# Kernel optimization log

Measured on AMD Instinct MI355X. Metric: run time of the kernel, lower is better.

The kernel has to match this reference:

```python
import jax, jax.numpy as jnp
import numpy as np

D_MODEL = 1024
D_STATE = 16
EXPAND = 2
D_INNER = D_MODEL * EXPAND
DT_RANK = D_MODEL // 16


def setup_inputs() -> dict:
    key = jax.random.key(0)
    ks = jax.random.split(key, 12)
    B, T = 2, 2048
    s_in = 1.0 / np.sqrt(D_MODEL)
    s_x = 1.0 / np.sqrt(D_INNER)
    s_dt = 1.0 / np.sqrt(DT_RANK)
    inp = {
        'u': jax.random.normal(ks[0], (B, T, D_MODEL), jnp.float32),
        'W_in': jax.random.uniform(ks[1], (2 * D_INNER, D_MODEL), jnp.float32, -s_in, s_in),
        'b_in': jax.random.uniform(ks[2], (2 * D_INNER,), jnp.float32, -s_in, s_in),
        'W_x': jax.random.uniform(ks[3], (DT_RANK + 2 * D_STATE, D_INNER), jnp.float32, -s_x, s_x),
        'b_x': jax.random.uniform(ks[4], (DT_RANK + 2 * D_STATE,), jnp.float32, -s_x, s_x),
        'W_dt': jax.random.uniform(ks[5], (D_INNER, DT_RANK), jnp.float32, -s_dt, s_dt),
        'b_dt': jax.random.uniform(ks[6], (D_INNER,), jnp.float32, -s_dt, s_dt),
        'A_log': jnp.log(jnp.abs(jax.random.normal(ks[7], (D_INNER, D_STATE), jnp.float32)) + 1e-6),
        'D': jnp.ones((D_INNER,), jnp.float32),
        'W_out': jax.random.uniform(ks[8], (D_MODEL, D_INNER), jnp.float32, -s_x, s_x),
        'b_out': jax.random.uniform(ks[9], (D_MODEL,), jnp.float32, -s_x, s_x),
    }
    return inp


def _ssm_forward(u, W_in, b_in, W_x, b_x, W_dt, b_dt, A_log, D, W_out, b_out):
    B, T, _ = u.shape
    u_inner = u @ W_in.T + b_in                       # [B,T,2*d_inner]
    x, z = jnp.split(u_inner, 2, axis=-1)             # each [B,T,d_inner]
    dbc = x @ W_x.T + b_x                             # [B,T,dt_rank+2N]
    delta_raw = dbc[..., :DT_RANK]
    B_ssm = dbc[..., DT_RANK:DT_RANK + D_STATE]       # [B,T,N]
    C_ssm = dbc[..., DT_RANK + D_STATE:]              # [B,T,N]
    delta = jax.nn.softplus(delta_raw @ W_dt.T + b_dt)  # [B,T,d_inner]
    A = -jnp.exp(A_log)                               # [d_inner,N]

    def step(h, xs):
        dt_t, x_t, Bt, Ct = xs                        # [B,d], [B,d], [B,N], [B,N]
        dA = jnp.exp(dt_t[..., None] * A)             # [B,d,N]
        dB = dt_t[..., None] * Bt[:, None, :]         # [B,d,N]
        h = h * dA + x_t[..., None] * dB
        y_t = jnp.einsum('bdn,bn->bd', h, Ct)
        return h, y_t

    h0 = jnp.zeros((B, D_INNER, D_STATE), u.dtype)
    xs = (jnp.swapaxes(delta, 0, 1), jnp.swapaxes(x, 0, 1),
          jnp.swapaxes(B_ssm, 0, 1), jnp.swapaxes(C_ssm, 0, 1))
    _, y = jax.lax.scan(step, h0, xs)                 # y: [T,B,d_inner]
    y = jnp.swapaxes(y, 0, 1)                         # [B,T,d_inner]
    y = y + x * D
    y = y * (z * jax.nn.sigmoid(z))                   # SiLU gate
    return y @ W_out.T + b_out                        # [B,T,d_model]


def reference(u, W_in, b_in, W_x, b_x, W_dt, b_dt, A_log, D, W_out, b_out):
    return _ssm_forward(u, W_in, b_in, W_x, b_x, W_dt, b_dt, A_log, D, W_out, b_out)
```

## Files before the change

### kernel.cpp

```cpp
#include <hip/hip_runtime.h>
#include <math.h>

#define BATCH 2
#define SEQ   2048
#define DM    1024
#define DI    2048
#define NST   16
#define MT    (BATCH*SEQ)
#define CHK   64
#define LCH   (SEQ/CHK)

typedef __attribute__((ext_vector_type(8))) short  bf16x8;
typedef __attribute__((ext_vector_type(4))) float  f32x4;

static __device__ __forceinline__ unsigned short f2bf(float f) {
  unsigned u = __float_as_uint(f);
  u += 0x7fff + ((u >> 16) & 1);
  return (unsigned short)(u >> 16);
}
static __device__ __forceinline__ float bf2f(unsigned short h) {
  return __uint_as_float(((unsigned)h) << 16);
}
static __device__ __forceinline__ float fexp2(float x) {
  float r;
  asm("v_exp_f32 %0, %1" : "=v"(r) : "v"(x));
  return r;
}
static __device__ __forceinline__ float flog2(float x) {
  float r;
  asm("v_log_f32 %0, %1" : "=v"(r) : "v"(x));
  return r;
}

#define SEG_U    (MT*DM/4)
#define SEG_WIN  (2*DI*DM/4)
#define SEG_WOUT (DM*DI/4)
#define SEG_WX   (96*DI/4)
#define SEG_WDT  (DI*64/4)
#define SEG_A    (DI*NST/4)
#define CUM0 SEG_U
#define CUM1 (CUM0+SEG_WIN)
#define CUM2 (CUM1+SEG_WOUT)
#define CUM3 (CUM2+SEG_WX)
#define CUM4 (CUM3+SEG_WDT)
#define CUM5 (CUM4+SEG_A)

__global__ __launch_bounds__(256) void convall_kernel(
    const float* __restrict__ u, const float* __restrict__ W_in,
    const float* __restrict__ W_out, const float* __restrict__ W_x,
    const float* __restrict__ W_dt, const float* __restrict__ A_log,
    unsigned short* __restrict__ u_bf, unsigned short* __restrict__ win_bf,
    unsigned short* __restrict__ wout_bf, unsigned short* __restrict__ wx_bf,
    unsigned short* __restrict__ wdt_bf, float* __restrict__ A2tab)
{
  const int gid = blockIdx.x*256 + threadIdx.x;
  const float4* src; ushort4* dst; int idx;
  if (gid < CUM0)      { idx = gid;        src = (const float4*)u;     dst = (ushort4*)u_bf; }
  else if (gid < CUM1) { idx = gid - CUM0; src = (const float4*)W_in;  dst = (ushort4*)win_bf; }
  else if (gid < CUM2) { idx = gid - CUM1; src = (const float4*)W_out; dst = (ushort4*)wout_bf; }
  else if (gid < CUM3) { idx = gid - CUM2; src = (const float4*)W_x;   dst = (ushort4*)wx_bf; }
  else if (gid < CUM4) { idx = gid - CUM3; src = (const float4*)W_dt;  dst = (ushort4*)wdt_bf; }
  else if (gid < CUM5) {
    int i = gid - CUM4;
    float4 v = ((const float4*)A_log)[i];
    float4 o;
    o.x = -1.44269504f * __expf(v.x);
    o.y = -1.44269504f * __expf(v.y);
    o.z = -1.44269504f * __expf(v.z);
    o.w = -1.44269504f * __expf(v.w);
    ((float4*)A2tab)[i] = o;
    return;
  } else return;
  float4 v = src[idx];
  ushort4 o;
  o.x = f2bf(v.x); o.y = f2bf(v.y); o.z = f2bf(v.z); o.w = f2bf(v.w);
  dst[idx] = o;
}

#define MEMFENCE asm volatile("" ::: "memory")

template<int K>
__global__ __launch_bounds__(512, 2) void gemm3_kernel(
    const unsigned short* __restrict__ A,
    const unsigned short* __restrict__ B,
    const float* __restrict__ bias,
    unsigned short* __restrict__ Cout, int nbx)
{
  extern __shared__ unsigned short smem[];
  unsigned short* As = smem;
  unsigned short* Bs = smem + 4*256*32;
  constexpr int NT = K / 32;

  const int nwg = gridDim.x;
  const int cpx = nwg >> 3;
  const int bid = blockIdx.x;
  const int swz = (bid & 7) * cpx + (bid >> 3);
  const int bx = swz % nbx;
  const int by = swz / nbx;

  const int tid  = threadIdx.x;
  const int lane = tid & 63;
  const int wid  = tid >> 6;
  const int wr   = wid >> 2;
  const int wc   = wid & 3;

  const size_t arow0 = (size_t)by * 256;
  const size_t brow0 = (size_t)bx * 256;

  const int s_r4 = lane >> 2;
  const int s_c  = lane & 3;

  auto STAGE_A = [&](int slot, int T) {
#pragma unroll
    for (int i = 0; i < 2; ++i) {
      const int r  = wid*32 + i*16 + s_r4;
      const int lc = s_c ^ ((r >> 1) & 3);
      const unsigned short* g = A + (arow0 + r)*(size_t)K + T*32 + lc*8;
      __builtin_amdgcn_global_load_lds(
          (const __attribute__((address_space(1))) void*)g,
          (__attribute__((address_space(3))) void*)(As + slot*(256*32) + (wid*32 + i*16)*32),
          16, 0, 0);
    }
  };
  auto STAGE_B = [&](int slot, int T) {
#pragma unroll
    for (int i = 0; i < 2; ++i) {
      const int r  = wid*32 + i*16 + s_r4;
      const int lc = s_c ^ ((r >> 1) & 3);
      const unsigned short* g = B + (brow0 + r)*(size_t)K + T*32 + lc*8;
      __builtin_amdgcn_global_load_lds(
          (const __attribute__((address_space(1))) void*)g,
          (__attribute__((address_space(3))) void*)(Bs + slot*(256*32) + (wid*32 + i*16)*32),
          16, 0, 0);
    }
  };

  f32x4 zero = {0.f, 0.f, 0.f, 0.f};
  f32x4 acc[8][4];
#pragma unroll
  for (int i = 0; i < 8; ++i)
#pragma unroll
    for (int j = 0; j < 4; ++j) acc[i][j] = zero;

  STAGE_A(0, 0); STAGE_B(0, 0);
  STAGE_A(1, 1); STAGE_B(1, 1);
  STAGE_A(2, 2); STAGE_B(2, 2);
  asm volatile("s_waitcnt vmcnt(8)" ::: "memory");
  __builtin_amdgcn_s_barrier();
  MEMFENCE;

  const int lrow = lane & 15, k8 = lane >> 4;
  bf16x8 bfr[4];

  for (int t = 0; t < NT; ++t) {
    const int slot = t & 3;
    const int sts  = (t + 3) & 3;
    const unsigned short* Asl = As + slot*(256*32);
    const unsigned short* Bsl = Bs + slot*(256*32);

    bf16x8 af[4];
#pragma unroll
    for (int nj = 0; nj < 4; ++nj) {
      const int r = wc*64 + nj*16 + lrow;
      bfr[nj] = *(const bf16x8*)&Bsl[r*32 + (k8 ^ ((r >> 1) & 3))*8];
    }
#pragma unroll
    for (int mi = 0; mi < 4; ++mi) {
      const int r = wr*128 + mi*16 + lrow;
      af[mi] = *(const bf16x8*)&Asl[r*32 + (k8 ^ ((r >> 1) & 3))*8];
    }
    if (t + 3 < NT) STAGE_A(sts, t + 3);
    MEMFENCE;
    __builtin_amdgcn_s_barrier();
    MEMFENCE;
    __builtin_amdgcn_s_setprio(1);
#pragma unroll
    for (int mi = 0; mi < 4; ++mi)
#pragma unroll
      for (int nj = 0; nj < 4; ++nj)
        acc[mi][nj] = __builtin_amdgcn_mfma_f32_16x16x32_bf16(
                          af[mi], bfr[nj], acc[mi][nj], 0, 0, 0);
    __builtin_amdgcn_s_setprio(0);
    MEMFENCE;
    __builtin_amdgcn_s_barrier();
    MEMFENCE;

#pragma unroll
    for (int mi = 0; mi < 4; ++mi) {
      const int r = wr*128 + 64 + mi*16 + lrow;
      af[mi] = *(const bf16x8*)&Asl[r*32 + (k8 ^ ((r >> 1) & 3))*8];
    }
    if (t + 3 < NT) STAGE_B(sts, t + 3);
    MEMFENCE;
    __builtin_amdgcn_s_barrier();
    MEMFENCE;
    __builtin_amdgcn_s_setprio(1);
#pragma unroll
    for (int mi = 0; mi < 4; ++mi)
#pragma unroll
      for (int nj = 0; nj < 4; ++nj)
        acc[mi + 4][nj] = __builtin_amdgcn_mfma_f32_16x16x32_bf16(
                              af[mi], bfr[nj], acc[mi + 4][nj], 0, 0, 0);
    __builtin_amdgcn_s_setprio(0);

    if (t <= NT - 4)      asm volatile("s_waitcnt vmcnt(8)" ::: "memory");
    else if (t == NT - 3) asm volatile("s_waitcnt vmcnt(4)" ::: "memory");
    else                  asm volatile("s_waitcnt vmcnt(0)" ::: "memory");
    __builtin_amdgcn_s_barrier();
    MEMFENCE;
  }

  const int lcol = lane & 15, lrq = lane >> 4;
#pragma unroll
  for (int nj = 0; nj < 4; ++nj) {
    const int colg = bx*256 + wc*64 + nj*16 + lcol;
    const float bv = bias[colg];
#pragma unroll
    for (int mi = 0; mi < 8; ++mi) {
      const int rowg = by*256 + wr*128 + mi*16 + lrq*4;
#pragma unroll
      for (int q = 0; q < 4; ++q)
        Cout[(size_t)(rowg + q)*4096 + colg] = f2bf(acc[mi][nj][q] + bv);
    }
  }
}

template<int BN, int BK, bool OUT_BF16, int LDC, int ACT>
__global__ __launch_bounds__(256, 4) void gemm2_kernel(
    const unsigned short* __restrict__ A,
    const unsigned short* __restrict__ B,
    const float* __restrict__ bias,
    void* __restrict__ Cout, int K, int nbx)
{
  constexpr int NH = BK / 32;
  constexpr int NJ = BN / 32;
  __shared__ unsigned short Abuf[2][NH][128*32];
  __shared__ unsigned short Bbuf[2][NH][BN*32];

  const int nwg = gridDim.x;
  const int cpx = nwg >> 3;
  const int bid = blockIdx.x;
  const int swz = (bid & 7) * cpx + (bid >> 3);
  const int bx = swz % nbx;
  const int by = swz / nbx;

  const int tid  = threadIdx.x;
  const int lane = tid & 63;
  const int wid  = tid >> 6;
  const int wr   = wid >> 1;
  const int wc   = wid & 1;
  const int lr    = lane >> 2;
  const int lslot = lane & 3;

  f32x4 zero = {0.f, 0.f, 0.f, 0.f};
  f32x4 acc[4][NJ];
#pragma unroll
  for (int i = 0; i < 4; ++i)
#pragma unroll
    for (int j = 0; j < NJ; ++j) acc[i][j] = zero;

  const size_t arow0 = (size_t)by * 128;
  const size_t brow0 = (size_t)bx * BN;
  const int NT = K / BK;

  auto STAGE = [&](int buf, int k0) {
#pragma unroll
    for (int half = 0; half < NH; ++half) {
#pragma unroll
      for (int i = 0; i < 2; ++i) {
        const int Rb = (wid + i*4) * 16;
        const int r  = Rb + lr;
        const int c8 = lslot ^ ((r >> 1) & 3);
        const unsigned short* ga = A + (arow0 + r)*(size_t)K + k0 + half*32 + c8*8;
        __builtin_amdgcn_global_load_lds(
            (const __attribute__((address_space(1))) void*)ga,
            (__attribute__((address_space(3))) void*)(&Abuf[buf][half][Rb*32]),
            16, 0, 0);
      }
#pragma unroll
      for (int i = 0; i < BN/64; ++i) {
        const int Rb = (wid + i*4) * 16;
        const int r  = Rb + lr;
        const int c8 = lslot ^ ((r >> 1) & 3);
        const unsigned short* gb = B + (brow0 + r)*(size_t)K + k0 + half*32 + c8*8;
        __builtin_amdgcn_global_load_lds(
            (const __attribute__((address_space(1))) void*)gb,
            (__attribute__((address_space(3))) void*)(&Bbuf[buf][half][Rb*32]),
            16, 0, 0);
      }
    }
  };

  STAGE(0, 0);
  __syncthreads();

  const int lrow = lane & 15, k8 = lane >> 4;
  int cur = 0;
  for (int kt = 0; kt < NT; ++kt) {
    if (kt + 1 < NT) STAGE(cur ^ 1, (kt + 1) * BK);

#pragma unroll
    for (int half = 0; half < NH; ++half) {
      bf16x8 af[4], bfr[NJ];
#pragma unroll
      for (int mi = 0; mi < 4; ++mi) {
        const int r = wr*64 + mi*16 + lrow;
        af[mi] = *(const bf16x8*)&Abuf[cur][half][r*32 + (k8 ^ ((r >> 1) & 3))*8];
      }
#pragma unroll
      for (int nj = 0; nj < NJ; ++nj) {
        const int r = wc*(BN/2) + nj*16 + lrow;
        bfr[nj] = *(const bf16x8*)&Bbuf[cur][half][r*32 + (k8 ^ ((r >> 1) & 3))*8];
      }
      __builtin_amdgcn_s_setprio(1);
#pragma unroll
      for (int mi = 0; mi < 4; ++mi)
#pragma unroll
        for (int nj = 0; nj < NJ; ++nj)
          acc[mi][nj] = __builtin_amdgcn_mfma_f32_16x16x32_bf16(
                            af[mi], bfr[nj], acc[mi][nj], 0, 0, 0);
      __builtin_amdgcn_s_setprio(0);
    }
    __syncthreads();
    cur ^= 1;
  }

  const int lcol = lane & 15, lrq = lane >> 4;
#pragma unroll
  for (int nj = 0; nj < NJ; ++nj) {
    const int colg = bx*BN + wc*(BN/2) + nj*16 + lcol;
    const float bv = bias[colg];
#pragma unroll
    for (int mi = 0; mi < 4; ++mi) {
      const int rowg = by*128 + wr*64 + mi*16 + lrq*4;
#pragma unroll
      for (int q = 0; q < 4; ++q) {
        float v = acc[mi][nj][q] + bv;
        if constexpr (ACT == 1) {
          float e = fexp2(-1.44269504f * fabsf(v));
          v = fmaxf(v, 0.f) + 0.69314718f * flog2(1.f + e);
        }
        if constexpr (OUT_BF16)
          ((unsigned short*)Cout)[(size_t)(rowg + q)*LDC + colg] = f2bf(v);
        else
          ((float*)Cout)[(size_t)(rowg + q)*LDC + colg] = v;
      }
    }
  }
}

__global__ __launch_bounds__(256) void dbc_mfma_kernel(
    const unsigned short* __restrict__ A,
    const unsigned short* __restrict__ Bw,
    float* __restrict__ partial)
{
  __shared__ unsigned short Abuf[64*32];
  __shared__ unsigned short Bbuf[96*32];

  const int tid  = threadIdx.x;
  const int lane = tid & 63;
  const int wid  = tid >> 6;
  const int lr    = lane >> 2;
  const int lslot = lane & 3;
  const size_t arow0 = (size_t)blockIdx.x * 64;
  const int ks   = blockIdx.y;
  const int k0b  = ks * (DI/4);

  f32x4 zero = {0.f, 0.f, 0.f, 0.f};
  f32x4 acc[6];
#pragma unroll
  for (int j = 0; j < 6; ++j) acc[j] = zero;

  for (int k0 = k0b; k0 < k0b + DI/4; k0 += 32) {
    {
      const int Rb = wid*16;
      const int r  = Rb + lr;
      const int c8 = lslot ^ ((r >> 1) & 3);
      const unsigned short* ga = A + (arow0 + r)*4096 + k0 + c8*8;
      __builtin_amdgcn_global_load_lds(
          (const __attribute__((address_space(1))) void*)ga,
          (__attribute__((address_space(3))) void*)(Abuf + Rb*32), 16, 0, 0);
    }
    if (wid < 3) {
#pragma unroll
      for (int i = 0; i < 2; ++i) {
        const int Rb = wid*32 + i*16;
        const int r  = Rb + lr;
        const int c8 = lslot ^ ((r >> 1) & 3);
        const unsigned short* gb = Bw + (size_t)r*DI + k0 + c8*8;
        __builtin_amdgcn_global_load_lds(
            (const __attribute__((address_space(1))) void*)gb,
            (__attribute__((address_space(3))) void*)(Bbuf + Rb*32), 16, 0, 0);
      }
    }
    __syncthreads();

    const int lrow = lane & 15, k8 = lane >> 4;
    const int ra = wid*16 + lrow;
    bf16x8 af = *(const bf16x8*)&Abuf[ra*32 + (k8 ^ ((ra >> 1) & 3))*8];
#pragma unroll
    for (int nj = 0; nj < 6; ++nj) {
      const int rb = nj*16 + lrow;
      bf16x8 bf_ = *(const bf16x8*)&Bbuf[rb*32 + (k8 ^ ((rb >> 1) & 3))*8];
      acc[nj] = __builtin_amdgcn_mfma_f32_16x16x32_bf16(af, bf_, acc[nj], 0, 0, 0);
    }
    __syncthreads();
  }

  const int lcol = lane & 15, lrq = lane >> 4;
  const int rowg = (int)arow0 + wid*16 + lrq*4;
#pragma unroll
  for (int nj = 0; nj < 6; ++nj) {
    const int colg = nj*16 + lcol;
#pragma unroll
    for (int q = 0; q < 4; ++q)
      partial[((size_t)ks*MT + rowg + q)*96 + colg] = acc[nj][q];
  }
}

__global__ __launch_bounds__(256) void dbc_reduce_kernel(
    const float* __restrict__ partial, const float* __restrict__ bx,
    float* __restrict__ dbc, unsigned short* __restrict__ draw_bf)
{
  const int gid = blockIdx.x*256 + threadIdx.x;
  const int m = gid / 96;
  const int c = gid - m*96;
  const size_t stride = (size_t)MT*96;
  float s = partial[gid] + partial[gid + stride]
          + partial[gid + 2*stride] + partial[gid + 3*stride] + bx[c];
  if (c < 64) draw_bf[(size_t)m*64 + c] = f2bf(s);
  else        dbc[(size_t)m*96 + c] = s;
}

__global__ __launch_bounds__(256) void scanA_kernel(
    const unsigned short* __restrict__ uib,
    const float* __restrict__ dbc,
    const unsigned short* __restrict__ delta_bf,
    const float* __restrict__ A2tab,
    float* __restrict__ P,
    float* __restrict__ S)
{
  const int bid = blockIdx.x;
  const int d   = (bid & 7)*256 + threadIdx.x;
  const int c   = (bid >> 3) & (CHK-1);
  const int b   = bid >> 9;

  float A2[NST];
  {
    const float4* ap = (const float4*)(A2tab + (size_t)d*NST);
#pragma unroll
    for (int q = 0; q < 4; ++q) {
      float4 v = ap[q];
      A2[q*4+0] = v.x; A2[q*4+1] = v.y; A2[q*4+2] = v.z; A2[q*4+3] = v.w;
    }
  }

  float h[NST];
#pragma unroll
  for (int nn = 0; nn < NST; ++nn) h[nn] = 0.f;
  float sdt = 0.f;

  const int t0 = c * LCH;
  const unsigned short* dptr = delta_bf + ((size_t)b*SEQ + t0)*DI + d;
  const unsigned short* xptr = uib      + ((size_t)b*SEQ + t0)*4096 + d;
  const float* bptr          = dbc      + ((size_t)b*SEQ + t0)*96 + 64;

  float dt = bf2f(dptr[0]);
  float xv = bf2f(xptr[0]);
  float4 Bv0 = *(const float4*)(bptr + 0);
  float4 Bv1 = *(const float4*)(bptr + 4);
  float4 Bv2 = *(const float4*)(bptr + 8);
  float4 Bv3 = *(const float4*)(bptr + 12);

  for (int t = 0; t < LCH; ++t) {
    const float dtc = dt, xvc = xv;
    float Bc[NST] = {Bv0.x,Bv0.y,Bv0.z,Bv0.w, Bv1.x,Bv1.y,Bv1.z,Bv1.w,
                     Bv2.x,Bv2.y,Bv2.z,Bv2.w, Bv3.x,Bv3.y,Bv3.z,Bv3.w};
    if (t + 1 < LCH) {
      const size_t tn = (size_t)(t+1);
      dt = bf2f(dptr[tn*DI]);
      xv = bf2f(xptr[tn*4096]);
      const float* bp = bptr + tn*96;
      Bv0 = *(const float4*)(bp + 0);
      Bv1 = *(const float4*)(bp + 4);
      Bv2 = *(const float4*)(bp + 8);
      Bv3 = *(const float4*)(bp + 12);
    }
    sdt += dtc;
    const float xdt = xvc * dtc;
#pragma unroll
    for (int nn = 0; nn < NST; ++nn) {
      float dA = fexp2(dtc * A2[nn]);
      h[nn] = h[nn]*dA + xdt*Bc[nn];
    }
  }

  float* Pp = P + (((size_t)b*CHK + c)*DI + d)*NST;
  float* Sp = S + (((size_t)b*CHK + c)*DI + d)*NST;
#pragma unroll
  for (int q = 0; q < 4; ++q) {
    float4 pv = { fexp2(A2[q*4+0]*sdt), fexp2(A2[q*4+1]*sdt),
                  fexp2(A2[q*4+2]*sdt), fexp2(A2[q*4+3]*sdt) };
    float4 sv = { h[q*4+0], h[q*4+1], h[q*4+2], h[q*4+3] };
    *(float4*)(Pp + q*4) = pv;
    *(float4*)(Sp + q*4) = sv;
  }
}

__global__ __launch_bounds__(256) void scanB_kernel(
    const float* __restrict__ P, float* __restrict__ S)
{
  const int gid = blockIdx.x*256 + threadIdx.x;
  const int n4 = gid & 3;
  const int d  = (gid >> 2) & (DI-1);
  const int b  = gid >> 13;

  float4 h = {0.f, 0.f, 0.f, 0.f};
  for (int c = 0; c < CHK; ++c) {
    const size_t idx = (((size_t)b*CHK + c)*DI + d)*NST + n4*4;
    float4 p = *(const float4*)(P + idx);
    float4 s = *(const float4*)(S + idx);
    *(float4*)(S + idx) = h;
    h.x = h.x*p.x + s.x;
    h.y = h.y*p.y + s.y;
    h.z = h.z*p.z + s.z;
    h.w = h.w*p.w + s.w;
  }
}

__global__ __launch_bounds__(256) void scanC_kernel(
    const unsigned short* __restrict__ uib,
    const float* __restrict__ dbc,
    const unsigned short* __restrict__ delta_bf,
    const float* __restrict__ A2tab,
    const float* __restrict__ Dp,
    const float* __restrict__ S,
    unsigned short* __restrict__ y_bf)
{
  const int bid = blockIdx.x;
  const int d   = (bid & 7)*256 + threadIdx.x;
  const int c   = (bid >> 3) & (CHK-1);
  const int b   = bid >> 9;

  float A2[NST];
  {
    const float4* ap = (const float4*)(A2tab + (size_t)d*NST);
#pragma unroll
    for (int q = 0; q < 4; ++q) {
      float4 v = ap[q];
      A2[q*4+0] = v.x; A2[q*4+1] = v.y; A2[q*4+2] = v.z; A2[q*4+3] = v.w;
    }
  }
  const float Dv = Dp[d];

  float h[NST];
  {
    const float* Sp = S + (((size_t)b*CHK + c)*DI + d)*NST;
#pragma unroll
    for (int q = 0; q < 4; ++q) {
      float4 sv = *(const float4*)(Sp + q*4);
      h[q*4+0] = sv.x; h[q*4+1] = sv.y; h[q*4+2] = sv.z; h[q*4+3] = sv.w;
    }
  }

  const int t0 = c * LCH;
  const unsigned short* dptr = delta_bf + ((size_t)b*SEQ + t0)*DI + d;
  const unsigned short* xptr = uib      + ((size_t)b*SEQ + t0)*4096 + d;
  const float* cptr          = dbc      + ((size_t)b*SEQ + t0)*96;
  unsigned short* yp         = y_bf     + ((size_t)b*SEQ + t0)*DI + d;

  float dt = bf2f(dptr[0]);
  float xv = bf2f(xptr[0]);
  float zv = bf2f(xptr[2048]);
  float4 Bv0 = *(const float4*)(cptr + 64);
  float4 Bv1 = *(const float4*)(cptr + 68);
  float4 Bv2 = *(const float4*)(cptr + 72);
  float4 Bv3 = *(const float4*)(cptr + 76);
  float4 Cv0 = *(const float4*)(cptr + 80);
  float4 Cv1 = *(const float4*)(cptr + 84);
  float4 Cv2 = *(const float4*)(cptr + 88);
  float4 Cv3 = *(const float4*)(cptr + 92);

  for (int t = 0; t < LCH; ++t) {
    const float dtc = dt, xvc = xv, zvc = zv;
    float Bc[NST] = {Bv0.x,Bv0.y,Bv0.z,Bv0.w, Bv1.x,Bv1.y,Bv1.z,Bv1.w,
                     Bv2.x,Bv2.y,Bv2.z,Bv2.w, Bv3.x,Bv3.y,Bv3.z,Bv3.w};
    float Cc[NST] = {Cv0.x,Cv0.y,Cv0.z,Cv0.w, Cv1.x,Cv1.y,Cv1.z,Cv1.w,
                     Cv2.x,Cv2.y,Cv2.z,Cv2.w, Cv3.x,Cv3.y,Cv3.z,Cv3.w};
    if (t + 1 < LCH) {
      const size_t tn = (size_t)(t+1);
      dt = bf2f(dptr[tn*DI]);
      xv = bf2f(xptr[tn*4096]);
      zv = bf2f(xptr[tn*4096 + 2048]);
      const float* cp = cptr + tn*96;
      Bv0 = *(const float4*)(cp + 64);
      Bv1 = *(const float4*)(cp + 68);
      Bv2 = *(const float4*)(cp + 72);
      Bv3 = *(const float4*)(cp + 76);
      Cv0 = *(const float4*)(cp + 80);
      Cv1 = *(const float4*)(cp + 84);
      Cv2 = *(const float4*)(cp + 88);
      Cv3 = *(const float4*)(cp + 92);
    }
    const float xdt = xvc * dtc;
    float y = 0.f;
#pragma unroll
    for (int nn = 0; nn < NST; ++nn) {
      float dA = fexp2(dtc * A2[nn]);
      h[nn] = h[nn]*dA + xdt*Bc[nn];
      y += h[nn]*Cc[nn];
    }
    y += xvc * Dv;
    y *= zvc / (1.f + fexp2(-1.44269504f * zvc));
    yp[(size_t)t*DI] = f2bf(y);
  }
}

extern "C" void kernel_launch(void* const* d_in, const int* in_sizes, int n_in,
                              void* d_out, int out_size, void* d_ws, size_t ws_size,
                              hipStream_t stream)
{
  const float* u     = (const float*)d_in[0];
  const float* W_in  = (const float*)d_in[1];
  const float* b_in  = (const float*)d_in[2];
  const float* W_x   = (const float*)d_in[3];
  const float* b_x   = (const float*)d_in[4];
  const float* W_dt  = (const float*)d_in[5];
  const float* b_dt  = (const float*)d_in[6];
  const float* A_log = (const float*)d_in[7];
  const float* Dp    = (const float*)d_in[8];
  const float* W_out = (const float*)d_in[9];
  const float* b_out = (const float*)d_in[10];
  float* out = (float*)d_out;

  unsigned short* ui_bf    = (unsigned short*)d_ws;
  float*          dbc      = (float*)(ui_bf + (size_t)MT*4096);
  unsigned short* delta_bf = (unsigned short*)(dbc + (size_t)MT*96);
  unsigned short* y_bf     = delta_bf + (size_t)MT*DI;
  unsigned short* wout_bf  = y_bf + (size_t)MT*DI;
  unsigned short* wx_bf    = wout_bf + (size_t)DM*DI;
  unsigned short* wdt_bf   = wx_bf + (size_t)96*DI;
  unsigned short* draw_bf  = wdt_bf + (size_t)DI*64;
  float*          S        = (float*)(draw_bf + (size_t)MT*64);
  float*          A2tab    = S + (size_t)BATCH*CHK*DI*NST;
  float*          partial  = A2tab + (size_t)DI*NST;

  unsigned short* u_bf   = (unsigned short*)d_out;
  unsigned short* win_bf = u_bf + (size_t)MT*DM;
  float* P = (float*)d_out;

  convall_kernel<<<CUM5/256, 256, 0, stream>>>(
      u, W_in, W_out, W_x, W_dt, A_log,
      u_bf, win_bf, wout_bf, wx_bf, wdt_bf, A2tab);

  bool big = hipFuncSetAttribute(
      (const void*)gemm3_kernel<DM>,
      hipFuncAttributeMaxDynamicSharedMemorySize, 131072) == hipSuccess;
  if (big) {
    gemm3_kernel<DM><<<16*16, 512, 131072, stream>>>(
        u_bf, win_bf, b_in, ui_bf, 16);
  } else {
    gemm2_kernel<128, 32, true, 4096, 0><<<32*32, 256, 0, stream>>>(
        u_bf, win_bf, b_in, ui_bf, DM, 32);
  }

  dbc_mfma_kernel<<<dim3(MT/64, 4), 256, 0, stream>>>(ui_bf, wx_bf, partial);
  dbc_reduce_kernel<<<MT*96/256, 256, 0, stream>>>(partial, b_x, dbc, draw_bf);

  gemm2_kernel<128, 32, true, 2048, 1><<<16*32, 256, 0, stream>>>(
      draw_bf, wdt_bf, b_dt, delta_bf, 64, 16);

  scanA_kernel<<<BATCH*CHK*DI/256, 256, 0, stream>>>(ui_bf, dbc, delta_bf, A2tab, P, S);
  scanB_kernel<<<BATCH*DI*4/256, 256, 0, stream>>>(P, S);
  scanC_kernel<<<BATCH*CHK*DI/256, 256, 0, stream>>>(ui_bf, dbc, delta_bf, A2tab, Dp, S, y_bf);

  gemm2_kernel<64, 64, false, 1024, 0><<<16*32, 256, 0, stream>>>(
      y_bf, wout_bf, b_out, out, DI, 16);
}
```

Measured before the change: 185.5 us.

## Split-K the output projection GEMM and drop intermediate barriers in gemm3

The output projection now runs as a two-way split-K GEMM with 128x128 tiles. Each K half writes fp32 partials into workspace reused from the dead u_inner buffer, and a new vectorised kernel sums the halves and adds the bias. Separately, the mid-iteration LDS barriers in the main input GEMM are removed, keeping only the end-of-iteration barrier, to cut synchronisation stalls. The split-K path adds an extra round trip of fp32 partials through global memory. The barrier removal leans on the 4-slot ring buffer spacing to stay race-free.

```diff
diff --git a/kernel.cpp b/kernel.cpp
--- a/kernel.cpp
+++ b/kernel.cpp
@@ -171,8 +171,6 @@
     }
     if (t + 3 < NT) STAGE_A(sts, t + 3);
     MEMFENCE;
-    __builtin_amdgcn_s_barrier();
-    MEMFENCE;
     __builtin_amdgcn_s_setprio(1);
 #pragma unroll
     for (int mi = 0; mi < 4; ++mi)
@@ -182,8 +180,6 @@
                           af[mi], bfr[nj], acc[mi][nj], 0, 0, 0);
     __builtin_amdgcn_s_setprio(0);
     MEMFENCE;
-    __builtin_amdgcn_s_barrier();
-    MEMFENCE;
 
 #pragma unroll
     for (int mi = 0; mi < 4; ++mi) {
@@ -191,8 +187,6 @@
       af[mi] = *(const bf16x8*)&Asl[r*32 + (k8 ^ ((r >> 1) & 3))*8];
     }
     if (t + 3 < NT) STAGE_B(sts, t + 3);
-    MEMFENCE;
-    __builtin_amdgcn_s_barrier();
     MEMFENCE;
     __builtin_amdgcn_s_setprio(1);
 #pragma unroll
@@ -225,7 +219,7 @@
   }
 }
 
-template<int BN, int BK, bool OUT_BF16, int LDC, int ACT>
+template<int BN, int BK, bool OUT_BF16, int LDC, int ACT, bool SPLITK = false>
 __global__ __launch_bounds__(256, 4) void gemm2_kernel(
     const unsigned short* __restrict__ A,
     const unsigned short* __restrict__ B,
@@ -243,6 +237,9 @@
   const int swz = (bid & 7) * cpx + (bid >> 3);
   const int bx = swz % nbx;
   const int by = swz / nbx;
+
+  const int stride = SPLITK ? 2*K : K;
+  const int koff   = SPLITK ? blockIdx.y * K : 0;
 
   const int tid  = threadIdx.x;
   const int lane = tid & 63;
@@ -271,7 +268,7 @@
         const int Rb = (wid + i*4) * 16;
         const int r  = Rb + lr;
         const int c8 = lslot ^ ((r >> 1) & 3);
-        const unsigned short* ga = A + (arow0 + r)*(size_t)K + k0 + half*32 + c8*8;
+        const unsigned short* ga = A + (arow0 + r)*(size_t)stride + koff + k0 + half*32 + c8*8;
         __builtin_amdgcn_global_load_lds(
             (const __attribute__((address_space(1))) void*)ga,
             (__attribute__((address_space(3))) void*)(&Abuf[buf][half][Rb*32]),
@@ -282,7 +279,7 @@
         const int Rb = (wid + i*4) * 16;
         const int r  = Rb + lr;
         const int c8 = lslot ^ ((r >> 1) & 3);
-        const unsigned short* gb = B + (brow0 + r)*(size_t)K + k0 + half*32 + c8*8;
+        const unsigned short* gb = B + (brow0 + r)*(size_t)stride + koff + k0 + half*32 + c8*8;
         __builtin_amdgcn_global_load_lds(
             (const __attribute__((address_space(1))) void*)gb,
             (__attribute__((address_space(3))) void*)(&Bbuf[buf][half][Rb*32]),
@@ -326,10 +323,12 @@
   }
 
   const int lcol = lane & 15, lrq = lane >> 4;
+  float* outp = (float*)Cout;
+  if constexpr (SPLITK) outp += (size_t)blockIdx.y * MT * LDC;
 #pragma unroll
   for (int nj = 0; nj < NJ; ++nj) {
     const int colg = bx*BN + wc*(BN/2) + nj*16 + lcol;
-    const float bv = bias[colg];
+    const float bv = SPLITK ? 0.f : bias[colg];
 #pragma unroll
     for (int mi = 0; mi < 4; ++mi) {
       const int rowg = by*128 + wr*64 + mi*16 + lrq*4;
@@ -343,10 +342,23 @@
         if constexpr (OUT_BF16)
           ((unsigned short*)Cout)[(size_t)(rowg + q)*LDC + colg] = f2bf(v);
         else
-          ((float*)Cout)[(size_t)(rowg + q)*LDC + colg] = v;
+          outp[(size_t)(rowg + q)*LDC + colg] = v;
       }
     }
   }
+}
+
+__global__ __launch_bounds__(256) void out_reduce_kernel(
+    const float* __restrict__ part, const float* __restrict__ bias,
+    float* __restrict__ out)
+{
+  const int gid = blockIdx.x*256 + threadIdx.x;
+  const int c4  = gid & (DM/4 - 1);
+  float4 p0 = ((const float4*)part)[gid];
+  float4 p1 = ((const float4*)part)[gid + MT*DM/4];
+  float4 bv = ((const float4*)bias)[c4];
+  float4 o = { p0.x+p1.x+bv.x, p0.y+p1.y+bv.y, p0.z+p1.z+bv.z, p0.w+p1.w+bv.w };
+  ((float4*)out)[gid] = o;
 }
 
 __global__ __launch_bounds__(256) void dbc_mfma_kernel(
@@ -648,6 +660,7 @@
   unsigned short* u_bf   = (unsigned short*)d_out;
   unsigned short* win_bf = u_bf + (size_t)MT*DM;
   float* P = (float*)d_out;
+  float* pK = (float*)d_ws;
 
   convall_kernel<<<CUM5/256, 256, 0, stream>>>(
       u, W_in, W_out, W_x, W_dt, A_log,
@@ -674,6 +687,7 @@
   scanB_kernel<<<BATCH*DI*4/256, 256, 0, stream>>>(P, S);
   scanC_kernel<<<BATCH*CHK*DI/256, 256, 0, stream>>>(ui_bf, dbc, delta_bf, A2tab, Dp, S, y_bf);
 
-  gemm2_kernel<64, 64, false, 1024, 0><<<16*32, 256, 0, stream>>>(
-      y_bf, wout_bf, b_out, out, DI, 16);
-}
+  gemm2_kernel<128, 32, false, 1024, 0, true><<<dim3(8*32, 2), 256, 0, stream>>>(
+      y_bf, wout_bf, nullptr, pK, 1024, 8);
+  out_reduce_kernel<<<MT*DM/4/256, 256, 0, stream>>>(pK, b_out, out);
+}
```

Measured after the change: 193.5 us. +4.3%, slower.

## Drop intra-iteration GEMM barriers and stage scan B/C vectors in LDS

Applied to the files above, without the earlier changes.

Removes three of the four per-iteration workgroup barriers in the GEMM main loop, leaving only the end-of-iteration barrier after the vmcnt wait, to reduce synchronisation stalls between the LDS fragment reads, stage loads and MFMA phases. The scan kernels now load each chunk's B (and C) vectors into shared memory once per block instead of having every thread issue per-timestep global float4 loads, so they become LDS broadcast reads. Removing the barriers risks races: next-stage global-to-LDS writes can overlap with other waves' fragment reads, so correctness depends on the 4-slot ring spacing being sufficient.

```diff
diff --git a/kernel.cpp b/kernel.cpp
--- a/kernel.cpp
+++ b/kernel.cpp
@@ -171,8 +171,6 @@
     }
     if (t + 3 < NT) STAGE_A(sts, t + 3);
     MEMFENCE;
-    __builtin_amdgcn_s_barrier();
-    MEMFENCE;
     __builtin_amdgcn_s_setprio(1);
 #pragma unroll
     for (int mi = 0; mi < 4; ++mi)
@@ -182,8 +180,6 @@
                           af[mi], bfr[nj], acc[mi][nj], 0, 0, 0);
     __builtin_amdgcn_s_setprio(0);
     MEMFENCE;
-    __builtin_amdgcn_s_barrier();
-    MEMFENCE;
 
 #pragma unroll
     for (int mi = 0; mi < 4; ++mi) {
@@ -191,8 +187,6 @@
       af[mi] = *(const bf16x8*)&Asl[r*32 + (k8 ^ ((r >> 1) & 3))*8];
     }
     if (t + 3 < NT) STAGE_B(sts, t + 3);
-    MEMFENCE;
-    __builtin_amdgcn_s_barrier();
     MEMFENCE;
     __builtin_amdgcn_s_setprio(1);
 #pragma unroll
@@ -440,10 +434,21 @@
     float* __restrict__ P,
     float* __restrict__ S)
 {
+  __shared__ float Bsh[LCH][16];
   const int bid = blockIdx.x;
   const int d   = (bid & 7)*256 + threadIdx.x;
   const int c   = (bid >> 3) & (CHK-1);
   const int b   = bid >> 9;
+  const int t0  = c * LCH;
+
+  {
+    int i = threadIdx.x;
+    if (i < LCH*4) {
+      int st = i >> 2, p = i & 3;
+      float4 v = *(const float4*)(dbc + ((size_t)b*SEQ + t0 + st)*96 + 64 + p*4);
+      *(float4*)&Bsh[st][p*4] = v;
+    }
+  }
 
   float A2[NST];
   {
@@ -460,32 +465,26 @@
   for (int nn = 0; nn < NST; ++nn) h[nn] = 0.f;
   float sdt = 0.f;
 
-  const int t0 = c * LCH;
   const unsigned short* dptr = delta_bf + ((size_t)b*SEQ + t0)*DI + d;
   const unsigned short* xptr = uib      + ((size_t)b*SEQ + t0)*4096 + d;
-  const float* bptr          = dbc      + ((size_t)b*SEQ + t0)*96 + 64;
 
   float dt = bf2f(dptr[0]);
   float xv = bf2f(xptr[0]);
-  float4 Bv0 = *(const float4*)(bptr + 0);
-  float4 Bv1 = *(const float4*)(bptr + 4);
-  float4 Bv2 = *(const float4*)(bptr + 8);
-  float4 Bv3 = *(const float4*)(bptr + 12);
+  __syncthreads();
 
   for (int t = 0; t < LCH; ++t) {
     const float dtc = dt, xvc = xv;
-    float Bc[NST] = {Bv0.x,Bv0.y,Bv0.z,Bv0.w, Bv1.x,Bv1.y,Bv1.z,Bv1.w,
-                     Bv2.x,Bv2.y,Bv2.z,Bv2.w, Bv3.x,Bv3.y,Bv3.z,Bv3.w};
     if (t + 1 < LCH) {
       const size_t tn = (size_t)(t+1);
       dt = bf2f(dptr[tn*DI]);
       xv = bf2f(xptr[tn*4096]);
-      const float* bp = bptr + tn*96;
-      Bv0 = *(const float4*)(bp + 0);
-      Bv1 = *(const float4*)(bp + 4);
-      Bv2 = *(const float4*)(bp + 8);
-      Bv3 = *(const float4*)(bp + 12);
-    }
+    }
+    float4 Bv0 = *(const float4*)&Bsh[t][0];
+    float4 Bv1 = *(const float4*)&Bsh[t][4];
+    float4 Bv2 = *(const float4*)&Bsh[t][8];
+    float4 Bv3 = *(const float4*)&Bsh[t][12];
+    float Bc[NST] = {Bv0.x,Bv0.y,Bv0.z,Bv0.w, Bv1.x,Bv1.y,Bv1.z,Bv1.w,
+                     Bv2.x,Bv2.y,Bv2.z,Bv2.w, Bv3.x,Bv3.y,Bv3.z,Bv3.w};
     sdt += dtc;
     const float xdt = xvc * dtc;
 #pragma unroll
@@ -537,10 +536,19 @@
     const float* __restrict__ S,
     unsigned short* __restrict__ y_bf)
 {
+  __shared__ float BCs[LCH][32];
   const int bid = blockIdx.x;
   const int d   = (bid & 7)*256 + threadIdx.x;
   const int c   = (bid >> 3) & (CHK-1);
   const int b   = bid >> 9;
+  const int t0  = c * LCH;
+
+  {
+    int i = threadIdx.x;
+    int st = i >> 3, p = i & 7;
+    float4 v = *(const float4*)(dbc + ((size_t)b*SEQ + t0 + st)*96 + 64 + p*4);
+    *(float4*)&BCs[st][p*4] = v;
+  }
 
   float A2[NST];
   {
@@ -563,45 +571,35 @@
     }
   }
 
-  const int t0 = c * LCH;
   const unsigned short* dptr = delta_bf + ((size_t)b*SEQ + t0)*DI + d;
   const unsigned short* xptr = uib      + ((size_t)b*SEQ + t0)*4096 + d;
-  const float* cptr          = dbc      + ((size_t)b*SEQ + t0)*96;
   unsigned short* yp         = y_bf     + ((size_t)b*SEQ + t0)*DI + d;
 
   float dt = bf2f(dptr[0]);
   float xv = bf2f(xptr[0]);
   float zv = bf2f(xptr[2048]);
-  float4 Bv0 = *(const float4*)(cptr + 64);
-  float4 Bv1 = *(const float4*)(cptr + 68);
-  float4 Bv2 = *(const float4*)(cptr + 72);
-  float4 Bv3 = *(const float4*)(cptr + 76);
-  float4 Cv0 = *(const float4*)(cptr + 80);
-  float4 Cv1 = *(const float4*)(cptr + 84);
-  float4 Cv2 = *(const float4*)(cptr + 88);
-  float4 Cv3 = *(const float4*)(cptr + 92);
+  __syncthreads();
 
   for (int t = 0; t < LCH; ++t) {
     const float dtc = dt, xvc = xv, zvc = zv;
-    float Bc[NST] = {Bv0.x,Bv0.y,Bv0.z,Bv0.w, Bv1.x,Bv1.y,Bv1.z,Bv1.w,
-                     Bv2.x,Bv2.y,Bv2.z,Bv2.w, Bv3.x,Bv3.y,Bv3.z,Bv3.w};
-    float Cc[NST] = {Cv0.x,Cv0.y,Cv0.z,Cv0.w, Cv1.x,Cv1.y,Cv1.z,Cv1.w,
-                     Cv2.x,Cv2.y,Cv2.z,Cv2.w, Cv3.x,Cv3.y,Cv3.z,Cv3.w};
     if (t + 1 < LCH) {
       const size_t tn = (size_t)(t+1);
       dt = bf2f(dptr[tn*DI]);
       xv = bf2f(xptr[tn*4096]);
       zv = bf2f(xptr[tn*4096 + 2048]);
-      const float* cp = cptr + tn*96;
-      Bv0 = *(const float4*)(cp + 64);
-      Bv1 = *(const float4*)(cp + 68);
-      Bv2 = *(const float4*)(cp + 72);
-      Bv3 = *(const float4*)(cp + 76);
-      Cv0 = *(const float4*)(cp + 80);
-      Cv1 = *(const float4*)(cp + 84);
-      Cv2 = *(const float4*)(cp + 88);
-      Cv3 = *(const float4*)(cp + 92);
-    }
+    }
+    float4 Bv0 = *(const float4*)&BCs[t][0];
+    float4 Bv1 = *(const float4*)&BCs[t][4];
+    float4 Bv2 = *(const float4*)&BCs[t][8];
+    float4 Bv3 = *(const float4*)&BCs[t][12];
+    float4 Cv0 = *(const float4*)&BCs[t][16];
+    float4 Cv1 = *(const float4*)&BCs[t][20];
+    float4 Cv2 = *(const float4*)&BCs[t][24];
+    float4 Cv3 = *(const float4*)&BCs[t][28];
+    float Bc[NST] = {Bv0.x,Bv0.y,Bv0.z,Bv0.w, Bv1.x,Bv1.y,Bv1.z,Bv1.w,
+                     Bv2.x,Bv2.y,Bv2.z,Bv2.w, Bv3.x,Bv3.y,Bv3.z,Bv3.w};
+    float Cc[NST] = {Cv0.x,Cv0.y,Cv0.z,Cv0.w, Cv1.x,Cv1.y,Cv1.z,Cv1.w,
+                     Cv2.x,Cv2.y,Cv2.z,Cv2.w, Cv3.x,Cv3.y,Cv3.z,Cv3.w};
     const float xdt = xvc * dtc;
     float y = 0.f;
 #pragma unroll
```

Measured after the change: 183.3 us, median of 2. No clear change (-1.2%).
